# Performance work log

Measured on AMD Instinct MI355X. Metric: run time of the kernel, lower is better.

Reference implementation:

```python
import jax, jax.numpy as jnp
import numpy as np

Z, N, K, W = 131072, 64, 64, 32


def setup_inputs() -> dict:
    key = jax.random.key(0)
    k1, k2, k3 = jax.random.split(key, 3)
    features = jax.random.normal(k1, (Z, N), dtype=jnp.float32)
    # dense realization of the CG-derived mixing tensor 'wkij'
    mixing_matrix = jax.random.normal(k2, (W, K, N, N), dtype=jnp.float32) * 0.05
    weight = jax.random.normal(k3, (W,), dtype=jnp.float32)
    return {"features": features, "mixing_matrix": mixing_matrix, "weight": weight}


def reference(features, mixing_matrix, weight):
    # torch: einsum('w,wkij,zi,zj->zk', weight, mixing_matrix, features, features)
    # Contract the small path axis w first -> [K, N, N] (cheap, tiny output),
    # then the bilinear square over z. einsum chooses a GEMM-style path; the
    # [Z, N, N] outer-product side is the memory-bound part.
    M = jnp.einsum('w,wkij->kij', weight, mixing_matrix)  # [K, N, N]
    out = jnp.einsum('kij,zi,zj->zk', M, features, features)  # [Z, K]
    return out
```

## Files before the change

### kernel.cpp

```cpp
#include <hip/hip_runtime.h>
#include <stdint.h>

typedef __attribute__((ext_vector_type(8))) _Float16 half8;
typedef __attribute__((ext_vector_type(2))) _Float16 h2;
typedef __attribute__((ext_vector_type(4))) float f32x4;

#define NCHUNK 32

static __device__ __forceinline__ unsigned short f2h(float f) {
  return __builtin_bit_cast(unsigned short, (_Float16)f);
}
static __device__ __forceinline__ float h2f_(unsigned short s) {
  return (float)__builtin_bit_cast(_Float16, s);
}
static __device__ __forceinline__ void gload16(const void* g, void* l) {
  __builtin_amdgcn_global_load_lds((const __attribute__((address_space(1))) void*)g,
                                   (__attribute__((address_space(3))) void*)l, 16, 0, 0);
}

__global__ __launch_bounds__(256) void prep_kernel(const float* __restrict__ mix,
                                                   const float* __restrict__ wgt,
                                                   unsigned short* __restrict__ Bp) {
  __shared__ float4 red[256];
  const int tid = threadIdx.x;
  const int ws  = tid >> 6;
  const int tt  = tid & 63;
  const int t4  = blockIdx.x * 64 + tt;
  const float4* m4 = (const float4*)mix;
  float ax = 0.f, ay = 0.f, az = 0.f, aw = 0.f;
#pragma unroll
  for (int wi = 0; wi < 8; ++wi) {
    const int w = ws * 8 + wi;
    const float s = wgt[w];
    const float4 v = m4[w * 65536 + t4];
    ax += s * v.x; ay += s * v.y; az += s * v.z; aw += s * v.w;
  }
  red[tid] = (float4){ax, ay, az, aw};
  __syncthreads();
  if (tid < 64) {
    const float4 a = red[tid], b = red[tid + 64], c = red[tid + 128], d = red[tid + 192];
    ushort4 r;
    r.x = f2h(a.x + b.x + c.x + d.x);
    r.y = f2h(a.y + b.y + c.y + d.y);
    r.z = f2h(a.z + b.z + c.z + d.z);
    r.w = f2h(a.w + b.w + c.w + d.w);
    ((ushort4*)Bp)[blockIdx.x * 64 + tid] = r;
  }
}

__global__ __launch_bounds__(256) void symm_kernel(unsigned short* __restrict__ Bp) {
  unsigned short* B = Bp + (size_t)blockIdx.x * 4096;
  for (int t = threadIdx.x; t < 4096; t += 256) {
    const int i = t >> 6, j = t & 63;
    if (i < j) {
      const int tt = (j << 6) | i;
      const float a = h2f_(B[t]);
      const float b = h2f_(B[tt]);
      B[t]  = f2h(a + b);
      B[tt] = 0;
    }
  }
}

__global__ __launch_bounds__(512, 4) void gemm_kernel(const float* __restrict__ X,
                                                      const unsigned short* __restrict__ Bp,
                                                      float* __restrict__ out) {
  __shared__ unsigned short ldsB[3][64 * 128];
  __shared__ unsigned short sH[2][2][256];

  const int tid  = threadIdx.x;
  const int lane = tid & 63;
  const int wv   = tid >> 6;
  const int wz   = wv >> 1;
  const int wk   = wv & 1;
  const int m    = lane & 15;
  const int q    = lane >> 4;
  const int zblk = blockIdx.x * 256;

  auto stageB = [&](int ct, int bf) {
#pragma unroll
    for (int it = 0; it < 2; ++it) {
      const int seg = wv * 2 + it;
      const int row = seg * 4 + (lane >> 4);
      const int u   = (lane & 15) ^ (row & 15);
      gload16(Bp + (size_t)row * 4096 + ct * 128 + u * 8,
              &ldsB[bf][seg * 512]);
    }
  };

  auto publishS = [&](int bf, float2 xp) {
    if (tid < 256) {
      const int d  = (tid >> 6) * 32 + (tid & 15) * 2 + ((tid >> 5) & 1);
      const int hf = (tid >> 4) & 1;
      sH[bf][0][d * 2 + hf] = f2h(xp.x);
      sH[bf][1][d * 2 + hf] = f2h(xp.y);
    }
  };

  stageB(0, 0);
  stageB(1, 1);
  {
    float2 xp0 = {0.f, 0.f};
    if (tid < 256) xp0 = *(const float2*)(X + (size_t)(zblk + tid) * 64);
    publishS(0, xp0);
  }

  h2 jh[4][8];
  {
    const float4* X4g = (const float4*)X;
#pragma unroll
    for (int f = 0; f < 4; ++f) {
      const int zg = zblk + wz * 64 + f * 16 + m;
#pragma unroll
      for (int h = 0; h < 2; ++h) {
        const float4 a = X4g[zg * 16 + h * 8 + q * 2];
        const float4 b = X4g[zg * 16 + h * 8 + q * 2 + 1];
        jh[f][h * 4 + 0] = h2{(_Float16)a.x, (_Float16)a.y};
        jh[f][h * 4 + 1] = h2{(_Float16)a.z, (_Float16)a.w};
        jh[f][h * 4 + 2] = h2{(_Float16)b.x, (_Float16)b.y};
        jh[f][h * 4 + 3] = h2{(_Float16)b.z, (_Float16)b.w};
      }
    }
  }

  f32x4 acc[4][2];
#pragma unroll
  for (int f = 0; f < 4; ++f)
#pragma unroll
    for (int g = 0; g < 2; ++g) acc[f][g] = f32x4{0.f, 0.f, 0.f, 0.f};

  __syncthreads();

  int bufc = 0;
  for (int c = 0; c < NCHUNK; ++c) {
    const int cn = (c + 1) & (NCHUNK - 1);
    float2 spre = {0.f, 0.f};
    if (tid < 256)
      spre = *(const float2*)(X + (size_t)(zblk + tid) * 64 + cn * 2);
    int bs = bufc + 2; if (bs >= 3) bs -= 3;
    stageB((c + 2) & (NCHUNK - 1), bs);

    const unsigned short* Bl = &ldsB[bufc][0];
    const bool full = (c < 16);
#pragma unroll
    for (int il = 0; il < 2; ++il) {
      const uint2 sv = *(const uint2*)(&sH[c & 1][il][wz * 64 + m * 4]);
      h2 s2f[4];
      s2f[0] = __builtin_bit_cast(h2, __builtin_amdgcn_perm(sv.x, sv.x, 0x01000100u));
      s2f[1] = __builtin_bit_cast(h2, __builtin_amdgcn_perm(sv.x, sv.x, 0x03020302u));
      s2f[2] = __builtin_bit_cast(h2, __builtin_amdgcn_perm(sv.y, sv.y, 0x01000100u));
      s2f[3] = __builtin_bit_cast(h2, __builtin_amdgcn_perm(sv.y, sv.y, 0x03020302u));
      auto hblk = [&](int h) {
        const int u = ((il << 3) + (h << 2) + q) ^ m;
        const unsigned short* bb = Bl + (wk * 32 + m) * 128 + u * 8;
        const half8 b0 = *(const half8*)(const void*)(bb);
        const half8 b1 = *(const half8*)(const void*)(bb + 16 * 128);
#pragma unroll
        for (int f = 0; f < 4; ++f) {
          union { unsigned u[4]; half8 v; } A;
#pragma unroll
          for (int e = 0; e < 4; ++e) {
            const h2 pr = s2f[f] * jh[f][h * 4 + e];
            A.u[e] = __builtin_bit_cast(unsigned, pr);
          }
          acc[f][0] = __builtin_amdgcn_mfma_f32_16x16x32_f16(A.v, b0, acc[f][0], 0, 0, 0);
          acc[f][1] = __builtin_amdgcn_mfma_f32_16x16x32_f16(A.v, b1, acc[f][1], 0, 0, 0);
        }
      };
      if (full) hblk(0);
      hblk(1);
    }

    publishS(cn & 1, spre);
    asm volatile("s_waitcnt vmcnt(2)" ::: "memory");
    asm volatile("s_waitcnt lgkmcnt(0)" ::: "memory");
    __builtin_amdgcn_s_barrier();
    __builtin_amdgcn_sched_barrier(0);
    bufc = (bufc + 1 == 3) ? 0 : bufc + 1;
  }

#pragma unroll
  for (int f = 0; f < 4; ++f) {
    const int zr = zblk + wz * 64 + f * 16 + q * 4;
#pragma unroll
    for (int g = 0; g < 2; ++g)
#pragma unroll
      for (int r = 0; r < 4; ++r)
        out[(size_t)(zr + r) * 64 + wk * 32 + g * 16 + m] = acc[f][g][r];
  }
}

extern "C" void kernel_launch(void* const* d_in, const int* in_sizes, int n_in,
                              void* d_out, int out_size, void* d_ws, size_t ws_size,
                              hipStream_t stream) {
  const float* X   = (const float*)d_in[0];
  const float* mix = (const float*)d_in[1];
  const float* wgt = (const float*)d_in[2];
  float* out = (float*)d_out;
  unsigned short* Bp = (unsigned short*)d_ws;

  prep_kernel<<<1024, 256, 0, stream>>>(mix, wgt, Bp);
  symm_kernel<<<64, 256, 0, stream>>>(Bp);
  gemm_kernel<<<512, 512, 0, stream>>>(X, Bp, out);
}
```

Before: 161.1 us.

## Fuse symmetrization into prep kernel and add ping-pong barriers with priority in GEMM loop

The prep kernel now handles one k slice per 1024-thread block. It reduces over all 32 w values, stages the result in LDS and folds the upper and lower triangles there, which removes the separate symm kernel launch and its global round trip. In the GEMM main loop, the B fragments for each il half are loaded up front. Extra s_barrier / waitcnt pairs and s_setprio raise priority around the MFMA clusters, so waves alternate between memory and compute phases. This adds more barriers per chunk, which may cost sync overhead, and prep now runs only 64 blocks with a 32-deep serial reduction per thread.

```diff
diff --git a/kernel.cpp b/kernel.cpp
--- a/kernel.cpp
+++ b/kernel.cpp
@@ -10,56 +10,38 @@
 static __device__ __forceinline__ unsigned short f2h(float f) {
   return __builtin_bit_cast(unsigned short, (_Float16)f);
 }
-static __device__ __forceinline__ float h2f_(unsigned short s) {
-  return (float)__builtin_bit_cast(_Float16, s);
-}
 static __device__ __forceinline__ void gload16(const void* g, void* l) {
   __builtin_amdgcn_global_load_lds((const __attribute__((address_space(1))) void*)g,
                                    (__attribute__((address_space(3))) void*)l, 16, 0, 0);
 }
 
-__global__ __launch_bounds__(256) void prep_kernel(const float* __restrict__ mix,
-                                                   const float* __restrict__ wgt,
-                                                   unsigned short* __restrict__ Bp) {
-  __shared__ float4 red[256];
+__global__ __launch_bounds__(1024) void prep_kernel(const float* __restrict__ mix,
+                                                    const float* __restrict__ wgt,
+                                                    unsigned short* __restrict__ Bp) {
+  __shared__ float T[4096];
+  const int k   = blockIdx.x;
   const int tid = threadIdx.x;
-  const int ws  = tid >> 6;
-  const int tt  = tid & 63;
-  const int t4  = blockIdx.x * 64 + tt;
-  const float4* m4 = (const float4*)mix;
-  float ax = 0.f, ay = 0.f, az = 0.f, aw = 0.f;
-#pragma unroll
-  for (int wi = 0; wi < 8; ++wi) {
-    const int w = ws * 8 + wi;
+  const float4* m4 = (const float4*)mix + (size_t)k * 1024 + tid;
+  float4 a = {0.f, 0.f, 0.f, 0.f};
+#pragma unroll
+  for (int w = 0; w < 32; ++w) {
     const float s = wgt[w];
-    const float4 v = m4[w * 65536 + t4];
-    ax += s * v.x; ay += s * v.y; az += s * v.z; aw += s * v.w;
-  }
-  red[tid] = (float4){ax, ay, az, aw};
+    const float4 v = m4[(size_t)w * 65536];
+    a.x += s * v.x; a.y += s * v.y; a.z += s * v.z; a.w += s * v.w;
+  }
+  *(float4*)(&T[tid * 4]) = a;
   __syncthreads();
-  if (tid < 64) {
-    const float4 a = red[tid], b = red[tid + 64], c = red[tid + 128], d = red[tid + 192];
-    ushort4 r;
-    r.x = f2h(a.x + b.x + c.x + d.x);
-    r.y = f2h(a.y + b.y + c.y + d.y);
-    r.z = f2h(a.z + b.z + c.z + d.z);
-    r.w = f2h(a.w + b.w + c.w + d.w);
-    ((ushort4*)Bp)[blockIdx.x * 64 + tid] = r;
-  }
-}
-
-__global__ __launch_bounds__(256) void symm_kernel(unsigned short* __restrict__ Bp) {
-  unsigned short* B = Bp + (size_t)blockIdx.x * 4096;
-  for (int t = threadIdx.x; t < 4096; t += 256) {
-    const int i = t >> 6, j = t & 63;
-    if (i < j) {
-      const int tt = (j << 6) | i;
-      const float a = h2f_(B[t]);
-      const float b = h2f_(B[tt]);
-      B[t]  = f2h(a + b);
-      B[tt] = 0;
-    }
-  }
+  ushort4 r;
+#pragma unroll
+  for (int e = 0; e < 4; ++e) {
+    const int t = tid * 4 + e, i = t >> 6, j = t & 63;
+    float v;
+    if (i < j)       v = T[t] + T[(j << 6) | i];
+    else if (i == j) v = T[t];
+    else             v = 0.f;
+    ((unsigned short*)&r)[e] = f2h(v);
+  }
+  ((ushort4*)Bp)[k * 1024 + tid] = r;
 }
 
 __global__ __launch_bounds__(512, 4) void gemm_kernel(const float* __restrict__ X,
@@ -142,6 +124,7 @@
 
     const unsigned short* Bl = &ldsB[bufc][0];
     const bool full = (c < 16);
+
 #pragma unroll
     for (int il = 0; il < 2; ++il) {
       const uint2 sv = *(const uint2*)(&sH[c & 1][il][wz * 64 + m * 4]);
@@ -150,11 +133,24 @@
       s2f[1] = __builtin_bit_cast(h2, __builtin_amdgcn_perm(sv.x, sv.x, 0x03020302u));
       s2f[2] = __builtin_bit_cast(h2, __builtin_amdgcn_perm(sv.y, sv.y, 0x01000100u));
       s2f[3] = __builtin_bit_cast(h2, __builtin_amdgcn_perm(sv.y, sv.y, 0x03020302u));
-      auto hblk = [&](int h) {
-        const int u = ((il << 3) + (h << 2) + q) ^ m;
-        const unsigned short* bb = Bl + (wk * 32 + m) * 128 + u * 8;
-        const half8 b0 = *(const half8*)(const void*)(bb);
-        const half8 b1 = *(const half8*)(const void*)(bb + 16 * 128);
+      const unsigned short* base = Bl + (wk * 32 + m) * 128;
+      const int u0 = ((il << 3) + q) ^ m;
+      const int u1 = ((il << 3) + 4 + q) ^ m;
+      half8 bf[2][2];
+      if (full) {
+        bf[0][0] = *(const half8*)(const void*)(base + u0 * 8);
+        bf[0][1] = *(const half8*)(const void*)(base + 16 * 128 + u0 * 8);
+      }
+      bf[1][0] = *(const half8*)(const void*)(base + u1 * 8);
+      bf[1][1] = *(const half8*)(const void*)(base + 16 * 128 + u1 * 8);
+      __builtin_amdgcn_sched_barrier(0);
+
+      __builtin_amdgcn_s_barrier();
+      asm volatile("s_waitcnt lgkmcnt(0)" ::: "memory");
+      __builtin_amdgcn_sched_barrier(0);
+
+      __builtin_amdgcn_s_setprio(1);
+      auto cluster = [&](int h, half8 b0, half8 b1) {
 #pragma unroll
         for (int f = 0; f < 4; ++f) {
           union { unsigned u[4]; half8 v; } A;
@@ -167,15 +163,18 @@
           acc[f][1] = __builtin_amdgcn_mfma_f32_16x16x32_f16(A.v, b1, acc[f][1], 0, 0, 0);
         }
       };
-      if (full) hblk(0);
-      hblk(1);
-    }
-
-    publishS(cn & 1, spre);
-    asm volatile("s_waitcnt vmcnt(2)" ::: "memory");
-    asm volatile("s_waitcnt lgkmcnt(0)" ::: "memory");
-    __builtin_amdgcn_s_barrier();
-    __builtin_amdgcn_sched_barrier(0);
+      if (full) cluster(0, bf[0][0], bf[0][1]);
+      cluster(1, bf[1][0], bf[1][1]);
+      __builtin_amdgcn_s_setprio(0);
+
+      if (il == 1) {
+        publishS(cn & 1, spre);
+        asm volatile("s_waitcnt vmcnt(2)" ::: "memory");
+        asm volatile("s_waitcnt lgkmcnt(0)" ::: "memory");
+      }
+      __builtin_amdgcn_s_barrier();
+      __builtin_amdgcn_sched_barrier(0);
+    }
     bufc = (bufc + 1 == 3) ? 0 : bufc + 1;
   }
 
@@ -199,7 +198,6 @@
   float* out = (float*)d_out;
   unsigned short* Bp = (unsigned short*)d_ws;
 
-  prep_kernel<<<1024, 256, 0, stream>>>(mix, wgt, Bp);
-  symm_kernel<<<64, 256, 0, stream>>>(Bp);
+  prep_kernel<<<64, 1024, 0, stream>>>(mix, wgt, Bp);
   gemm_kernel<<<512, 512, 0, stream>>>(X, Bp, out);
 }
```

New measurement: 164.2 us. Within noise of the previous version (+1.9%).
